# Kernel optimization log

Hardware: AMD Instinct MI355X
Metric: run time of the kernel (lower is better)

## Reference

```python
import jax, jax.numpy as jnp
import numpy as np

# Dimensions
B, T, IN = 8, 64, 6       # batch, timesteps, strain components
G = 256                   # grain_num
H = 32                    # hidden_dim (units)
W = 128                   # quadratic block width
OUT = 3                   # output_dim
DEPTH = 4                 # quadratic block depth
SD = H + IN               # start_dim = units + in_channels = 38
EPS = 1e-15


def setup_inputs() -> dict:
    key = jax.random.key(0)
    ks = jax.random.split(key, 24)
    s = 0.08  # xavier-ish scale for width-128 linears
    d = {
        "x": jax.random.normal(ks[0], (B, T, IN), dtype=jnp.float32),
        "init_ori": jax.random.normal(ks[1], (B, G, 3), dtype=jnp.float32),
        # Quadratic block branch A (modlist1): first layer SD->W, then (DEPTH-1) W->W
        "qbA_W0": jax.random.normal(ks[2], (SD, W)) * s,
        "qbA_b0": jnp.zeros((W,), jnp.float32),
        "qbA_Ws": jax.random.normal(ks[3], (DEPTH - 1, W, W)) * s,
        "qbA_bs": jnp.zeros((DEPTH - 1, W), jnp.float32),
        # Quadratic block branch B (modlist2)
        "qbB_W0": jax.random.normal(ks[4], (SD, W)) * s,
        "qbB_b0": jnp.zeros((W,), jnp.float32),
        "qbB_Ws": jax.random.normal(ks[5], (DEPTH - 1, W, W)) * s,
        "qbB_bs": jnp.zeros((DEPTH - 1, W), jnp.float32),
        # fc_alpha: W -> H ; fc_beta (1-layer DNN): W -> H
        "alpha_W": jax.random.normal(ks[6], (W, H)) * s,
        "alpha_b": jnp.zeros((H,), jnp.float32),
        "beta_W": jax.random.normal(ks[7], (W, H)) * s,
        "beta_b": jnp.zeros((H,), jnp.float32),
        # nn_out DNN: layers = [H, 128, 128, OUT], tanh between hidden layers
        "out_W0": jax.random.normal(ks[8], (H, 128)) * s,
        "out_b0": jnp.zeros((128,), jnp.float32),
        "out_W1": jax.random.normal(ks[9], (128, 128)) * s,
        "out_b1": jnp.zeros((128,), jnp.float32),
        "out_W2": jax.random.normal(ks[10], (128, OUT)) * s,
        "out_b2": jnp.zeros((OUT,), jnp.float32),
    }
    return d


def reference(x, init_ori, qbA_W0, qbA_b0, qbA_Ws, qbA_bs,
              qbB_W0, qbB_b0, qbB_Ws, qbB_bs,
              alpha_W, alpha_b, beta_W, beta_b,
              out_W0, out_b0, out_W1, out_b1, out_W2, out_b2):
    b = x.shape[0]
    # h0 = zeros with first 3 hidden channels set to initial orientations
    h0 = jnp.zeros((b, G, H), x.dtype).at[:, :, :3].set(init_ori)

    def step(h, x_t):  # h: [B,G,H], x_t: [B,IN]
        sn = jnp.linalg.norm(x_t, axis=-1, keepdims=True)          # [B,1]
        xn = x_t / (sn + EPS)                                      # normalized strain direction
        z = jnp.concatenate(
            [jnp.broadcast_to(xn[:, None, :], (b, G, IN)), h], axis=-1)  # [B,G,SD]
        # quadratic block: elementwise product of two linear branches
        a = jnp.tanh(z @ qbA_W0 + qbA_b0)
        c = jnp.tanh(z @ qbB_W0 + qbB_b0)
        z = a * c
        for j in range(DEPTH - 1):
            a = z @ qbA_Ws[j] + qbA_bs[j]
            c = z @ qbB_Ws[j] + qbB_bs[j]
            if j < DEPTH - 2:  # tanh on all but the last quadratic layer
                a = jnp.tanh(a)
                c = jnp.tanh(c)
            z = a * c
        q = jnp.tanh(z)                                            # [B,G,W]
        alpha = jnp.exp(q @ alpha_W + alpha_b)                     # [B,G,H]
        beta = jnp.tanh(q @ beta_W + beta_b)                       # [B,G,H]
        decay = jnp.exp(-alpha * sn[:, :, None])                   # exp(-alpha*||strain||)
        h_new = decay * (h - beta) + beta                          # gated state update
        # nn_out DNN [H,128,128,OUT] with tanh hidden activations
        o = jnp.tanh(h_new @ out_W0 + out_b0)
        o = jnp.tanh(o @ out_W1 + out_b1)
        o = o @ out_W2 + out_b2                                    # [B,G,OUT]
        return h_new, o

    _, outs = jax.lax.scan(step, h0, jnp.swapaxes(x, 0, 1))        # outs: [T,B,G,OUT]
    return jnp.transpose(outs, (1, 2, 0, 3))                       # [B,G,T,OUT]
```

## Files before the change

kernel.cpp:

```cpp
#include <hip/hip_runtime.h>

typedef _Float16 f16;
typedef _Float16 f16x4 __attribute__((ext_vector_type(4)));
typedef _Float16 f16x8 __attribute__((ext_vector_type(8)));
typedef float f32x4 __attribute__((ext_vector_type(4)));
typedef unsigned int u32;

#define MFMA16(a,b,c) __builtin_amdgcn_mfma_f32_16x16x32_f16(a,b,c,0,0,0)

#define BAR() asm volatile("s_waitcnt lgkmcnt(0)\n\ts_barrier" ::: "memory")

#define OFF_A0 0
#define OFF_B0 8192
#define OFF_AW 16384
#define OFF_BW 65536
#define OFF_AL 114688
#define OFF_BE 118784
#define OFF_O0 122880
#define OFF_O1 126976
#define OFF_O2 143360
#define PACK_TOTAL 145408
#define OFF_HH 262144

struct PackSrcs { const float* p[9]; };

__global__ __launch_bounds__(256) void pack_all(PackSrcs ps, f16* __restrict__ dst){
  int idx = blockIdx.x*256 + threadIdx.x;
  if (idx >= PACK_TOTAL) return;
  const float* src; int base, Kreal, Nreal, KT;
  if (idx < 16384){
    if (idx < 8192){ src=ps.p[0]; base=0; } else { src=ps.p[1]; base=8192; }
    Kreal=38; Nreal=128; KT=2;
  } else if (idx < 65536){
    int s=(idx-16384)>>14; src=ps.p[2]+s*16384; base=16384+s*16384; Kreal=128; Nreal=128; KT=4;
  } else if (idx < 114688){
    int s=(idx-65536)>>14; src=ps.p[3]+s*16384; base=65536+s*16384; Kreal=128; Nreal=128; KT=4;
  } else if (idx < 122880){
    if (idx<118784){ src=ps.p[4]; base=114688; } else { src=ps.p[5]; base=118784; }
    Kreal=128; Nreal=32; KT=4;
  } else if (idx < 126976){
    src=ps.p[6]; base=122880; Kreal=32; Nreal=128; KT=1;
  } else if (idx < 143360){
    src=ps.p[7]; base=126976; Kreal=128; Nreal=128; KT=4;
  } else {
    src=ps.p[8]; base=143360; Kreal=128; Nreal=3; KT=4;
  }
  int local = idx - base;
  int j = local & 7, lane = (local>>3)&63, rem = local>>9;
  int kt = rem % KT, nt = rem / KT;
  int k = kt*32 + ((lane>>4)<<3) + j;
  int n = nt*16 + (lane&15);
  if (base < 16384){
    k = (k < 32) ? (6 + ((k>>3)<<2) + (k&3) + ((k&4)<<2))
      : (k < 38) ? (k - 32) : 64;
  }
  dst[idx] = (f16)((k<Kreal && n<Nreal) ? src[k*Nreal+n] : 0.f);
}

__device__ __forceinline__ float tanhfast(float x){
  float e = __builtin_amdgcn_exp2f(x * 2.885390082f);
  return 1.f - 2.f*__builtin_amdgcn_rcpf(e + 1.f);
}
__device__ __forceinline__ float expfast(float x){
  return __builtin_amdgcn_exp2f(x * 1.44269504f);
}

__device__ __forceinline__ f16x8 ldW(const f16* wp, int off, int KT, int nt, int kt, int l){
  return *(const f16x8*)(wp + off + (((nt*KT + kt)*64 + l)<<3));
}

template<int LAST>
__device__ __forceinline__ void qphase(const f16* __restrict__ Zi, f16* __restrict__ Zo,
                                       const f16x8 (&WA)[4], const f16x8 (&WB)[4],
                                       const float* __restrict__ bA,
                                       const float* __restrict__ bB,
                                       int l, int d0, int n16){
  f16x8 Bq[4];
#pragma unroll
  for (int kt=0; kt<4; ++kt) Bq[kt] = *(const f16x8*)(Zi + ((kt*64 + l)<<3));
  f32x4 a = *(const f32x4*)(bA + d0);
  f32x4 c = *(const f32x4*)(bB + d0);
#pragma unroll
  for (int kt=0; kt<4; ++kt){
    a = MFMA16(WA[kt], Bq[kt], a);
    c = MFMA16(WB[kt], Bq[kt], c);
  }
  f16x4 z4;
#pragma unroll
  for (int i=0;i<4;++i){
    float z = LAST ? tanhfast(a[i]*c[i]) : tanhfast(a[i])*tanhfast(c[i]);
    z4[i] = (f16)z;
  }
  int kt_o = d0>>5, lane_o = (((d0&31)>>3)<<4) | n16, j0 = d0&7;
  *(f16x4*)(Zo + ((kt_o*64 + lane_o)<<3) + j0) = z4;
}

__global__ __launch_bounds__(512,2)
void lmsc_rec(const float* __restrict__ x, const float* __restrict__ init_ori,
              const f16* __restrict__ wp,
              const float* __restrict__ ba0, const float* __restrict__ bas,
              const float* __restrict__ bb0, const float* __restrict__ bbs,
              const float* __restrict__ b_al, const float* __restrict__ b_be,
              f16* __restrict__ hG)
{
  __shared__ __align__(16) f16 Z[2][2048];
  __shared__ float biasA[4][128], biasB[4][128], biasAB[64];
  __shared__ float dbuf[16*36], bbuf[16*36];
  __shared__ __align__(16) f16 xnH[64][8], xnL2[64][8];
  __shared__ float snS[64];

  const int tid = (int)threadIdx.x;
  const int l = tid & 63, wid = tid >> 6;
  const int n16 = l & 15, rhi = l >> 4;
  const int d0 = (wid<<4) + (rhi<<2);
  const int tile = (int)blockIdx.x, b = tile >> 4, Rbase = tile << 4;

  f16x8 w0A[2], w0B[2];
#pragma unroll
  for (int kt=0;kt<2;++kt){
    w0A[kt] = ldW(wp, OFF_A0, 2, wid, kt, l);
    w0B[kt] = ldW(wp, OFF_B0, 2, wid, kt, l);
  }
  f16x8 wqA[3][4], wqB[3][4];
#pragma unroll
  for (int ly=0;ly<3;++ly)
#pragma unroll
    for (int kt=0;kt<4;++kt){
      wqA[ly][kt] = ldW(wp, OFF_AW + ly*16384, 4, wid, kt, l);
      wqB[ly][kt] = ldW(wp, OFF_BW + ly*16384, 4, wid, kt, l);
    }
  f16x8 wab[4];
  if (wid < 4){
    const int offW = (wid<2)? OFF_AL : OFF_BE, tn = wid & 1;
#pragma unroll
    for (int kt=0;kt<4;++kt) wab[kt] = ldW(wp, offW, 4, tn, kt, l);
  }

  if (tid < 128){
    biasA[0][tid] = ba0[tid]; biasB[0][tid] = bb0[tid];
#pragma unroll
    for (int j=0;j<3;++j){ biasA[1+j][tid] = bas[j*128+tid]; biasB[1+j][tid] = bbs[j*128+tid]; }
  }
  if (tid < 32){ biasAB[tid] = b_al[tid]; biasAB[32+tid] = b_be[tid]; }
  if (tid < 64){
    const float* xp = x + (b*64 + tid)*6;
    float s2 = 0.f;
#pragma unroll
    for (int i=0;i<6;++i) s2 += xp[i]*xp[i];
    float sn = sqrtf(s2);
    float inv = 1.f/(sn + 1e-15f);
#pragma unroll
    for (int i=0;i<6;++i){
      float xv = xp[i]*inv;
      f16 xh = (f16)xv;
      xnH[tid][i] = xh; xnL2[tid][i] = (f16)(xv - (float)xh);
    }
    xnH[tid][6] = xnH[tid][7] = (f16)0.f;
    xnL2[tid][6] = xnL2[tid][7] = (f16)0.f;
    snS[tid] = -1.44269504f * sn;
  }

  float hreg[8];
#pragma unroll
  for (int j=0;j<8;++j) hreg[j] = 0.f;
  if (rhi == 0){
    const float* ip = init_ori + (Rbase + n16)*3;
    hreg[0] = ip[0]; hreg[1] = ip[1]; hreg[2] = ip[2];
  }
  __syncthreads();

  auto L0_step = [&](int tt){
    f16x8 Bh0, Bl0;
#pragma unroll
    for (int j=0;j<8;++j){
      f16 hh = (f16)hreg[j];
      Bh0[j] = hh;
      Bl0[j] = (f16)(hreg[j] - (float)hh);
    }
    f16x8 Bh1 = {0,0,0,0,0,0,0,0}, Bl1 = {0,0,0,0,0,0,0,0};
    if (rhi == 0){
      Bh1 = *(const f16x8*)(&xnH[tt][0]);
      Bl1 = *(const f16x8*)(&xnL2[tt][0]);
    }
    f32x4 aH = *(const f32x4*)(&biasA[0][d0]);
    f32x4 cH = *(const f32x4*)(&biasB[0][d0]);
    f32x4 aL = {0,0,0,0}, cL = {0,0,0,0};
    aH = MFMA16(w0A[0], Bh0, aH); aH = MFMA16(w0A[1], Bh1, aH);
    aL = MFMA16(w0A[0], Bl0, aL); aL = MFMA16(w0A[1], Bl1, aL);
    cH = MFMA16(w0B[0], Bh0, cH); cH = MFMA16(w0B[1], Bh1, cH);
    cL = MFMA16(w0B[0], Bl0, cL); cL = MFMA16(w0B[1], Bl1, cL);
    f16x4 z4;
#pragma unroll
    for (int i=0;i<4;++i)
      z4[i] = (f16)(tanhfast(aH[i]+aL[i]) * tanhfast(cH[i]+cL[i]));
    int kt_o = d0>>5, lane_o = (((d0&31)>>3)<<4) | n16, j0 = d0&7;
    *(f16x4*)(&Z[0][((kt_o*64 + lane_o)<<3) + j0]) = z4;
  };

  L0_step(0);
  BAR();

  for (int t=0; t<64; ++t){
    qphase<0>(Z[0], Z[1], wqA[0], wqB[0], biasA[1], biasB[1], l, d0, n16);
    BAR();
    qphase<0>(Z[1], Z[0], wqA[1], wqB[1], biasA[2], biasB[2], l, d0, n16);
    BAR();
    qphase<1>(Z[0], Z[1], wqA[2], wqB[2], biasA[3], biasB[3], l, d0, n16);
    BAR();
    if (wid < 4){
      f16x8 q[4];
#pragma unroll
      for (int kt=0;kt<4;++kt) q[kt] = *(const f16x8*)(&Z[1][(kt*64+l)<<3]);
      const int tn = wid & 1;
      f32x4 u = *(const f32x4*)(&biasAB[((wid>>1)<<5) + (tn<<4) + (rhi<<2)]);
#pragma unroll
      for (int kt=0;kt<4;++kt) u = MFMA16(wab[kt], q[kt], u);
      const int oi = n16*36 + (tn<<4) + (rhi<<2);
      if (wid < 2){
        float s2n = snS[t];
        f32x4 o;
#pragma unroll
        for (int i=0;i<4;++i){
          float alv = expfast(fminf(u[i], 80.f));
          o[i] = __builtin_amdgcn_exp2f(s2n * alv);
        }
        *(f32x4*)(&dbuf[oi]) = o;
      } else {
        f32x4 o;
#pragma unroll
        for (int i=0;i<4;++i) o[i] = tanhfast(u[i]);
        *(f32x4*)(&bbuf[oi]) = o;
      }
    }
    BAR();
    {
      const int gbase = n16*36 + (rhi<<2);
      f32x4 dlo = *(const f32x4*)(&dbuf[gbase]);
      f32x4 dhi = *(const f32x4*)(&dbuf[gbase+16]);
      f32x4 blo = *(const f32x4*)(&bbuf[gbase]);
      f32x4 bhi = *(const f32x4*)(&bbuf[gbase+16]);
#pragma unroll
      for (int i=0;i<4;++i){
        hreg[i]   = dlo[i]*(hreg[i]  -blo[i]) + blo[i];
        hreg[4+i] = dhi[i]*(hreg[4+i]-bhi[i]) + bhi[i];
      }
      if (wid == 2){
        int mt = tile*64 + t;
        f16x4 a4, b4;
#pragma unroll
        for (int i=0;i<4;++i){ a4[i]=(f16)hreg[i]; b4[i]=(f16)hreg[4+i]; }
        const int c0 = rhi<<2, c1 = 16 + (rhi<<2);
        f16* bp = hG + mt*512;
        *(f16x4*)(bp + (((c0>>3)<<4 | n16)<<3) + (c0&7)) = a4;
        *(f16x4*)(bp + (((c1>>3)<<4 | n16)<<3) + (c1&7)) = b4;
      }
      if (t < 63) L0_step(t+1);
    }
    BAR();
  }
}

__global__ __launch_bounds__(512,4)
void lmsc_out(const f16* __restrict__ wp, const f16* __restrict__ hG,
              const float* __restrict__ bo0, const float* __restrict__ bo1,
              const float* __restrict__ bo2, float* __restrict__ out)
{
  __shared__ __align__(16) f16 o1b[16384];
  __shared__ __align__(16) f16 o2b[16384];
  const int tid=(int)threadIdx.x, l=tid&63, wid=tid>>6;
  const int n16=l&15, rhi=l>>4;
  const int mtb = (int)blockIdx.x * 8;
  f16x8 W0a = ldW(wp, OFF_O0, 1, wid, 0, l);
  f16x8 W1a[4], W2a[4];
#pragma unroll
  for (int kt=0;kt<4;++kt){ W1a[kt]=ldW(wp,OFF_O1,4,wid,kt,l); W2a[kt]=ldW(wp,OFF_O2,4,0,kt,l); }
  const int d0 = wid*16 + rhi*4;
  const f32x4 b0v = *(const f32x4*)(bo0 + d0);
  const f32x4 b1v = *(const f32x4*)(bo1 + d0);
  const int kt_o = d0>>5, lane_o = (((d0&31)>>3)<<4) + n16, j0 = d0&7;
#pragma unroll
  for (int s=0;s<8;++s){
    int mt = mtb + s;
    f16x8 Bh = *(const f16x8*)(hG + ((mt*64+l)<<3));
    f32x4 acc = b0v;
    acc = MFMA16(W0a, Bh, acc);
    f16x4 z4;
#pragma unroll
    for (int i=0;i<4;++i) z4[i] = (f16)tanhfast(acc[i]);
    *(f16x4*)(&o1b[(((s*4+kt_o)*64 + lane_o)<<3) + j0]) = z4;
  }
  __syncthreads();
#pragma unroll
  for (int s=0;s<8;++s){
    f32x4 acc = b1v;
#pragma unroll
    for (int kt=0;kt<4;++kt){
      f16x8 B = *(const f16x8*)(&o1b[((s*4+kt)*64 + l)<<3]);
      acc = MFMA16(W1a[kt], B, acc);
    }
    f16x4 z4;
#pragma unroll
    for (int i=0;i<4;++i) z4[i] = (f16)tanhfast(acc[i]);
    *(f16x4*)(&o2b[(((s*4+kt_o)*64 + lane_o)<<3) + j0]) = z4;
  }
  __syncthreads();
  {
    f32x4 acc = {0,0,0,0};
#pragma unroll
    for (int kt=0;kt<4;++kt){
      f16x8 B = *(const f16x8*)(&o2b[((wid*4+kt)*64 + l)<<3]);
      acc = MFMA16(W2a[kt], B, acc);
    }
    if (l < 16){
      int mt = mtb + wid, grow = (mt>>6)*16 + n16, tt = mt & 63;
#pragma unroll
      for (int i=0;i<3;++i)
        out[(grow*64 + tt)*3 + i] = acc[i] + bo2[i];
    }
  }
}

extern "C" void kernel_launch(void* const* d_in, const int* in_sizes, int n_in,
                              void* d_out, int out_size, void* d_ws, size_t ws_size,
                              hipStream_t stream){
  const float* x        = (const float*)d_in[0];
  const float* init_ori = (const float*)d_in[1];
  f16* wp = (f16*)d_ws;

  PackSrcs ps;
  ps.p[0] = (const float*)d_in[2];
  ps.p[1] = (const float*)d_in[6];
  ps.p[2] = (const float*)d_in[4];
  ps.p[3] = (const float*)d_in[8];
  ps.p[4] = (const float*)d_in[10];
  ps.p[5] = (const float*)d_in[12];
  ps.p[6] = (const float*)d_in[14];
  ps.p[7] = (const float*)d_in[16];
  ps.p[8] = (const float*)d_in[18];
  pack_all<<<(PACK_TOTAL+255)/256, 256, 0, stream>>>(ps, wp);

  lmsc_rec<<<128,512,0,stream>>>(x, init_ori, wp,
      (const float*)d_in[3],  (const float*)d_in[5],
      (const float*)d_in[7],  (const float*)d_in[9],
      (const float*)d_in[11], (const float*)d_in[13],
      wp + OFF_HH);
  lmsc_out<<<1024,512,0,stream>>>(wp, wp + OFF_HH,
      (const float*)d_in[15], (const float*)d_in[17], (const float*)d_in[19],
      (float*)d_out);
}
```

Before: 146.3 us.

## Compute alpha/beta gates redundantly in every wave to drop a barrier

Every wave now loads all four alpha/beta weight tiles and runs the sixteen MFMAs itself, then applies the gated state update directly in registers. Previously four waves computed the gates, wrote them to shared-memory buffers, and a barrier was needed before all waves read them back. This removes one barrier and the LDS round trip on each of the 64 recurrent timesteps. In exchange it repeats the MFMA and transcendental work across all eight waves and holds sixteen more weight vectors in registers, which may hurt occupancy under launch_bounds(512,2).

After: 169.4 us. 15.8% more time.

```diff
diff --git a/kernel.cpp b/kernel.cpp
--- a/kernel.cpp
+++ b/kernel.cpp
@@ -105,7 +105,6 @@
 {
   __shared__ __align__(16) f16 Z[2][2048];
   __shared__ float biasA[4][128], biasB[4][128], biasAB[64];
-  __shared__ float dbuf[16*36], bbuf[16*36];
   __shared__ __align__(16) f16 xnH[64][8], xnL2[64][8];
   __shared__ float snS[64];
 
@@ -129,11 +128,13 @@
       wqA[ly][kt] = ldW(wp, OFF_AW + ly*16384, 4, wid, kt, l);
       wqB[ly][kt] = ldW(wp, OFF_BW + ly*16384, 4, wid, kt, l);
     }
-  f16x8 wab[4];
-  if (wid < 4){
-    const int offW = (wid<2)? OFF_AL : OFF_BE, tn = wid & 1;
-#pragma unroll
-    for (int kt=0;kt<4;++kt) wab[kt] = ldW(wp, offW, 4, tn, kt, l);
+  f16x8 wA0[4], wA1[4], wB0[4], wB1[4];
+#pragma unroll
+  for (int kt=0;kt<4;++kt){
+    wA0[kt] = ldW(wp, OFF_AL, 4, 0, kt, l);
+    wA1[kt] = ldW(wp, OFF_AL, 4, 1, kt, l);
+    wB0[kt] = ldW(wp, OFF_BE, 4, 0, kt, l);
+    wB1[kt] = ldW(wp, OFF_BE, 4, 1, kt, l);
   }
 
   if (tid < 128){
@@ -207,42 +208,33 @@
     BAR();
     qphase<1>(Z[0], Z[1], wqA[2], wqB[2], biasA[3], biasB[3], l, d0, n16);
     BAR();
-    if (wid < 4){
+    {
       f16x8 q[4];
 #pragma unroll
       for (int kt=0;kt<4;++kt) q[kt] = *(const f16x8*)(&Z[1][(kt*64+l)<<3]);
-      const int tn = wid & 1;
-      f32x4 u = *(const f32x4*)(&biasAB[((wid>>1)<<5) + (tn<<4) + (rhi<<2)]);
-#pragma unroll
-      for (int kt=0;kt<4;++kt) u = MFMA16(wab[kt], q[kt], u);
-      const int oi = n16*36 + (tn<<4) + (rhi<<2);
-      if (wid < 2){
-        float s2n = snS[t];
-        f32x4 o;
-#pragma unroll
-        for (int i=0;i<4;++i){
-          float alv = expfast(fminf(u[i], 80.f));
-          o[i] = __builtin_amdgcn_exp2f(s2n * alv);
-        }
-        *(f32x4*)(&dbuf[oi]) = o;
-      } else {
-        f32x4 o;
-#pragma unroll
-        for (int i=0;i<4;++i) o[i] = tanhfast(u[i]);
-        *(f32x4*)(&bbuf[oi]) = o;
+      const int rb = rhi<<2;
+      f32x4 uA0 = *(const f32x4*)(&biasAB[rb]);
+      f32x4 uA1 = *(const f32x4*)(&biasAB[16+rb]);
+      f32x4 uB0 = *(const f32x4*)(&biasAB[32+rb]);
+      f32x4 uB1 = *(const f32x4*)(&biasAB[48+rb]);
+#pragma unroll
+      for (int kt=0;kt<4;++kt){
+        uA0 = MFMA16(wA0[kt], q[kt], uA0);
+        uA1 = MFMA16(wA1[kt], q[kt], uA1);
+        uB0 = MFMA16(wB0[kt], q[kt], uB0);
+        uB1 = MFMA16(wB1[kt], q[kt], uB1);
       }
-    }
-    BAR();
-    {
-      const int gbase = n16*36 + (rhi<<2);
-      f32x4 dlo = *(const f32x4*)(&dbuf[gbase]);
-      f32x4 dhi = *(const f32x4*)(&dbuf[gbase+16]);
-      f32x4 blo = *(const f32x4*)(&bbuf[gbase]);
-      f32x4 bhi = *(const f32x4*)(&bbuf[gbase+16]);
+      const float snt = snS[t];
 #pragma unroll
       for (int i=0;i<4;++i){
-        hreg[i]   = dlo[i]*(hreg[i]  -blo[i]) + blo[i];
-        hreg[4+i] = dhi[i]*(hreg[4+i]-bhi[i]) + bhi[i];
+        float a0 = expfast(fminf(uA0[i], 80.f));
+        float a1 = expfast(fminf(uA1[i], 80.f));
+        float d0v = __builtin_amdgcn_exp2f(snt * a0);
+        float d1v = __builtin_amdgcn_exp2f(snt * a1);
+        float b0v = tanhfast(uB0[i]);
+        float b1v = tanhfast(uB1[i]);
+        hreg[i]   = d0v*(hreg[i]  -b0v) + b0v;
+        hreg[4+i] = d1v*(hreg[4+i]-b1v) + b1v;
       }
       if (wid == 2){
         int mt = tile*64 + t;
```
